# Optimization experiments

Measured on AMD Instinct MI355X. Metric: run time of the kernel, lower is better.

The kernel has to match this reference:

```python
import jax, jax.numpy as jnp
import numpy as np

B, F, CHUNK = 4096, 1024, 128  # batch, features, scan chunk size
EPS = 1e-5  # nn.LayerNorm default eps


def setup_inputs() -> dict:
    key = jax.random.key(0)
    k1, k2 = jax.random.split(key, 2)
    x = jax.random.normal(k1, (B, F), dtype=jnp.float32)
    W = jax.random.normal(k2, (F, F), dtype=jnp.float32) * 0.5  # init_weight = randn*0.5
    b = jnp.zeros((F,), dtype=jnp.float32)
    gamma = jnp.ones((F,), dtype=jnp.float32)   # LayerNorm weight
    beta = jnp.zeros((F,), dtype=jnp.float32)   # LayerNorm bias
    return {"x": x, "W": W, "b": b, "gamma": gamma, "beta": beta}


def reference(x, W, b, gamma, beta):
    # LayerNorm over last dim (biased variance, as torch)
    mu = jnp.mean(x, axis=-1, keepdims=True)
    var = jnp.mean(jnp.square(x - mu), axis=-1, keepdims=True)
    xn = (x - mu) * jax.lax.rsqrt(var + EPS) * gamma + beta  # [B, F]

    # Tropical max-plus matmul: out[b, i] = max_k xn[b, k] + W[k, i]
    # Chunk the batch to avoid materializing the full [B, F, F] broadcast-add.
    xc = xn.reshape(B // CHUNK, CHUNK, F)

    def step(_, xb):  # xb: [CHUNK, F]
        o = jnp.max(xb[:, :, None] + W[None, :, :], axis=1)  # [CHUNK, F]
        return None, o

    _, out = jax.lax.scan(step, None, xc)
    out = out.reshape(B, F)

    # Tropical bias: elementwise max with learned threshold b
    return jnp.maximum(out, b)
```

## Files before the change

kernel.cpp:

```cpp
#include <hip/hip_runtime.h>
#include <math.h>

#define F 1024
#define BM 256
#define BN 128
#define BK 16

typedef short s2 __attribute__((ext_vector_type(2)));
typedef short s4 __attribute__((ext_vector_type(4)));
typedef short s8 __attribute__((ext_vector_type(8)));
typedef float v4f __attribute__((ext_vector_type(4)));

#define SCALE 1024.0f
#define ISCALE (1.0f / 1024.0f)

static __device__ __forceinline__ s2 pk_max_i16(s2 a, s2 b) {
  s2 d;
  asm("v_pk_max_i16 %0, %1, %2" : "=v"(d) : "v"(a), "v"(b));
  return d;
}
static __device__ __forceinline__ s2 pk_add_blo(s2 a, s2 b) {
  s2 d;
  asm("v_pk_add_i16 %0, %1, %2 op_sel:[0,0] op_sel_hi:[0,1]" : "=v"(d) : "v"(a), "v"(b));
  return d;
}
static __device__ __forceinline__ s2 pk_add_bhi(s2 a, s2 b) {
  s2 d;
  asm("v_pk_add_i16 %0, %1, %2 op_sel:[1,0] op_sel_hi:[1,1]" : "=v"(d) : "v"(a), "v"(b));
  return d;
}

static __device__ __forceinline__ short q_i16(float v, float clampv) {
  return (short)__float2int_rn(fminf(fmaxf(v * SCALE, -clampv), clampv));
}

__global__ __launch_bounds__(256) void ln_kernel(const float* __restrict__ x,
                                                 const float* __restrict__ gamma,
                                                 const float* __restrict__ beta,
                                                 short* __restrict__ xn) {
  const int lane = threadIdx.x & 63;
  const int wv = threadIdx.x >> 6;
  const int row = blockIdx.x * 4 + wv;
  const float4* xr = (const float4*)(x + (size_t)row * F);
  float4 v[4];
  float s = 0.f;
#pragma unroll
  for (int j = 0; j < 4; ++j) {
    v[j] = xr[lane + 64 * j];
    s += v[j].x + v[j].y + v[j].z + v[j].w;
  }
#pragma unroll
  for (int off = 32; off; off >>= 1) s += __shfl_xor(s, off, 64);
  const float mu = s * (1.0f / F);
  float sq = 0.f;
#pragma unroll
  for (int j = 0; j < 4; ++j) {
    v[j].x -= mu; v[j].y -= mu; v[j].z -= mu; v[j].w -= mu;
    sq += v[j].x * v[j].x + v[j].y * v[j].y + v[j].z * v[j].z + v[j].w * v[j].w;
  }
#pragma unroll
  for (int off = 32; off; off >>= 1) sq += __shfl_xor(sq, off, 64);
  const float r = rsqrtf(sq * (1.0f / F) + 1e-5f);
  const float4* g4 = (const float4*)gamma;
  const float4* b4 = (const float4*)beta;
  s4* o = (s4*)(xn + (size_t)row * F);
#pragma unroll
  for (int j = 0; j < 4; ++j) {
    const int idx = lane + 64 * j;
    const float4 g = g4[idx];
    const float4 bb = b4[idx];
    s4 q;
    q[0] = q_i16(v[j].x * r * g.x + bb.x, 28000.f);
    q[1] = q_i16(v[j].y * r * g.y + bb.y, 28000.f);
    q[2] = q_i16(v[j].z * r * g.z + bb.z, 28000.f);
    q[3] = q_i16(v[j].w * r * g.w + bb.w, 28000.f);
    o[idx] = q;
  }
}

__global__ __launch_bounds__(256) void cvt_kernel(const float* __restrict__ Wf,
                                                  short* __restrict__ Wq) {
  const int i = blockIdx.x * 256 + threadIdx.x;
  const float4 v = ((const float4*)Wf)[i];
  s4 q;
  q[0] = q_i16(v.x, 4700.f);
  q[1] = q_i16(v.y, 4700.f);
  q[2] = q_i16(v.z, 4700.f);
  q[3] = q_i16(v.w, 4700.f);
  ((s4*)Wq)[i] = q;
}

__global__ __launch_bounds__(256, 2) void trop_i(const short* __restrict__ A,
                                                 const short* __restrict__ Wm,
                                                 const float* __restrict__ bias,
                                                 short* __restrict__ dsts,
                                                 float* __restrict__ outf,
                                                 int ntiles, int totrows, int fuse) {
  __shared__ alignas(16) short As[2][BK][BM];
  __shared__ alignas(16) short Bs[2][BK][BN];

  const int tid = threadIdx.x;
  const int tx = tid & 15;
  const int ty = tid >> 4;
  const int row0 = blockIdx.y * BM;
  const int col0 = blockIdx.x * BN;
  const int kbase = blockIdx.z * ntiles * BK;

  const int bk = tid >> 4;
  const int bn = (tid & 15) << 3;

  const short* Arow = A + (size_t)(row0 + tid) * F + kbase;
  const short* Wrow = Wm + (size_t)(kbase + bk) * F + col0 + bn;

  s2 acc[16][4];
  const s2 ninf = {(short)-32768, (short)-32768};
#pragma unroll
  for (int m = 0; m < 16; ++m)
#pragma unroll
    for (int n = 0; n < 4; ++n) acc[m][n] = ninf;

  {
    const s8 av0 = *(const s8*)Arow;
    const s8 av1 = *(const s8*)(Arow + 8);
    const s8 bv = *(const s8*)Wrow;
#pragma unroll
    for (int j = 0; j < 8; ++j) {
      As[0][j][tid] = av0[j];
      As[0][8 + j][tid] = av1[j];
    }
    *(s8*)&Bs[0][bk][bn] = bv;
  }
  __syncthreads();

  for (int kt = 0; kt < ntiles; ++kt) {
    const int cur = kt & 1;
    s8 av0, av1, bv;
    if (kt + 1 < ntiles) {
      const short* An = Arow + (kt + 1) * BK;
      av0 = *(const s8*)An;
      av1 = *(const s8*)(An + 8);
      bv = *(const s8*)(Wrow + (size_t)(kt + 1) * BK * F);
    }

#pragma unroll
    for (int k = 0; k < BK; ++k) {
      s8 alo = *(const s8*)&As[cur][k][ty * 16];
      s8 ahi = *(const s8*)&As[cur][k][ty * 16 + 8];
      s8 b = *(const s8*)&Bs[cur][k][tx * 8];
      const s2* al2 = (const s2*)&alo;
      const s2* ah2 = (const s2*)&ahi;
      const s2* b2 = (const s2*)&b;
#pragma unroll
      for (int m = 0; m < 8; ++m) {
        const s2 am = al2[m >> 1];
#pragma unroll
        for (int nn = 0; nn < 4; ++nn) {
          const s2 t = (m & 1) ? pk_add_bhi(am, b2[nn]) : pk_add_blo(am, b2[nn]);
          acc[m][nn] = pk_max_i16(acc[m][nn], t);
        }
      }
#pragma unroll
      for (int m = 0; m < 8; ++m) {
        const s2 am = ah2[m >> 1];
#pragma unroll
        for (int nn = 0; nn < 4; ++nn) {
          const s2 t = (m & 1) ? pk_add_bhi(am, b2[nn]) : pk_add_blo(am, b2[nn]);
          acc[8 + m][nn] = pk_max_i16(acc[8 + m][nn], t);
        }
      }
    }

    if (kt + 1 < ntiles) {
      const int nxt = cur ^ 1;
#pragma unroll
      for (int j = 0; j < 8; ++j) {
        As[nxt][j][tid] = av0[j];
        As[nxt][8 + j][tid] = av1[j];
      }
      *(s8*)&Bs[nxt][bk][bn] = bv;
      __syncthreads();
    }
  }

  if (fuse) {
    const float4 bv0 = *(const float4*)(bias + col0 + tx * 8);
    const float4 bv1 = *(const float4*)(bias + col0 + tx * 8 + 4);
#pragma unroll
    for (int m = 0; m < 16; ++m) {
      float* orow = outf + (size_t)(row0 + ty * 16 + m) * F + col0 + tx * 8;
      float4 o0, o1;
      o0.x = fmaxf((float)acc[m][0][0] * ISCALE, bv0.x);
      o0.y = fmaxf((float)acc[m][0][1] * ISCALE, bv0.y);
      o0.z = fmaxf((float)acc[m][1][0] * ISCALE, bv0.z);
      o0.w = fmaxf((float)acc[m][1][1] * ISCALE, bv0.w);
      o1.x = fmaxf((float)acc[m][2][0] * ISCALE, bv1.x);
      o1.y = fmaxf((float)acc[m][2][1] * ISCALE, bv1.y);
      o1.z = fmaxf((float)acc[m][3][0] * ISCALE, bv1.z);
      o1.w = fmaxf((float)acc[m][3][1] * ISCALE, bv1.w);
      *(float4*)orow = o0;
      *(float4*)(orow + 4) = o1;
    }
  } else {
    short* base = dsts + (size_t)blockIdx.z * totrows * F;
#pragma unroll
    for (int m = 0; m < 16; ++m) {
      short* orow = base + (size_t)(row0 + ty * 16 + m) * F + col0 + tx * 8;
      s8 o;
#pragma unroll
      for (int nn = 0; nn < 4; ++nn) {
        o[2 * nn] = acc[m][nn][0];
        o[2 * nn + 1] = acc[m][nn][1];
      }
      *(s8*)orow = o;
    }
  }
}

template <int NP>
__global__ __launch_bounds__(256) void combineNs(const short* __restrict__ p,
                                                 size_t plane,
                                                 const float* __restrict__ bias,
                                                 float* __restrict__ out) {
  const int i = blockIdx.x * 256 + threadIdx.x;
  s8 v = ((const s8*)p)[i];
  s2* vv = (s2*)&v;
#pragma unroll
  for (int q = 1; q < NP; ++q) {
    const s8 u = ((const s8*)(p + (size_t)q * plane))[i];
    const s2* uu = (const s2*)&u;
#pragma unroll
    for (int j = 0; j < 4; ++j) vv[j] = pk_max_i16(vv[j], uu[j]);
  }
  const int nb = (i & (F / 8 - 1)) * 8;
  const v4f bb0 = *(const v4f*)(bias + nb);
  const v4f bb1 = *(const v4f*)(bias + nb + 4);
  float4* o4 = (float4*)(out + (size_t)i * 8);
  float4 o0, o1;
  o0.x = fmaxf((float)v[0] * ISCALE, bb0.x);
  o0.y = fmaxf((float)v[1] * ISCALE, bb0.y);
  o0.z = fmaxf((float)v[2] * ISCALE, bb0.z);
  o0.w = fmaxf((float)v[3] * ISCALE, bb0.w);
  o1.x = fmaxf((float)v[4] * ISCALE, bb1.x);
  o1.y = fmaxf((float)v[5] * ISCALE, bb1.y);
  o1.z = fmaxf((float)v[6] * ISCALE, bb1.z);
  o1.w = fmaxf((float)v[7] * ISCALE, bb1.w);
  o4[0] = o0;
  o4[1] = o1;
}

extern "C" void kernel_launch(void* const* d_in, const int* in_sizes, int n_in,
                              void* d_out, int out_size, void* d_ws, size_t ws_size,
                              hipStream_t stream) {
  const float* x = (const float*)d_in[0];
  const float* Wm = (const float*)d_in[1];
  const float* bias = (const float*)d_in[2];
  const float* gamma = (const float*)d_in[3];
  const float* beta = (const float*)d_in[4];
  float* out = (float*)d_out;

  const int Brows = in_sizes[0] / F;
  const size_t plane = (size_t)Brows * F;

  short* xnq = (short*)d_ws;
  short* Wq = xnq + plane;
  short* parts = Wq + (size_t)F * F;

  ln_kernel<<<Brows / 4, 256, 0, stream>>>(x, gamma, beta, xnq);
  cvt_kernel<<<(F * F) / 1024, 256, 0, stream>>>(Wm, Wq);

  const size_t base2 = plane * 2 + (size_t)F * F * 2;
  const size_t need8 = base2 + 8 * plane * 2;
  const size_t need4 = base2 + 4 * plane * 2;
  const size_t need1 = base2;
  if (ws_size >= need8) {
    dim3 grid(F / BN, Brows / BM, 8);
    trop_i<<<grid, 256, 0, stream>>>(xnq, Wq, bias, parts, nullptr,
                                     (F / BK) / 8, Brows, 0);
    combineNs<8><<<(int)(plane / 2048), 256, 0, stream>>>(parts, plane, bias, out);
  } else if (ws_size >= need4) {
    dim3 grid(F / BN, Brows / BM, 4);
    trop_i<<<grid, 256, 0, stream>>>(xnq, Wq, bias, parts, nullptr,
                                     (F / BK) / 4, Brows, 0);
    combineNs<4><<<(int)(plane / 2048), 256, 0, stream>>>(parts, plane, bias, out);
  } else if (ws_size >= need1) {
    dim3 grid(F / BN, Brows / BM, 1);
    trop_i<<<grid, 256, 0, stream>>>(xnq, Wq, bias, nullptr, out, F / BK, Brows, 1);
  }
}
```

Measured before the change: 225.8 us.

## Transpose normalized activations and stage tiles via direct global-to-LDS loads

Adds a transpose kernel so the quantized activations are stored K-major. This lets the tropical matmul fill its shared-memory A and B tiles with global_load_lds 16-byte transfers, replacing register loads followed by scattered LDS stores. The goal is to cut register traffic and LDS store instructions in the main loop while keeping double buffering. The cost is an extra kernel launch, another pass over the activation plane, and a different workspace layout, with the partials buffer now aliasing the untransposed xn.

```diff
diff --git a/kernel.cpp b/kernel.cpp
--- a/kernel.cpp
+++ b/kernel.cpp
@@ -28,6 +28,12 @@
   s2 d;
   asm("v_pk_add_i16 %0, %1, %2 op_sel:[1,0] op_sel_hi:[1,1]" : "=v"(d) : "v"(a), "v"(b));
   return d;
+}
+
+static __device__ __forceinline__ void gll16(const short* src, short* lds) {
+  __builtin_amdgcn_global_load_lds(
+      (const __attribute__((address_space(1))) void*)src,
+      (__attribute__((address_space(3))) void*)lds, 16, 0, 0);
 }
 
 static __device__ __forceinline__ short q_i16(float v, float clampv) {
@@ -90,7 +96,32 @@
   ((s4*)Wq)[i] = q;
 }
 
-__global__ __launch_bounds__(256, 2) void trop_i(const short* __restrict__ A,
+__global__ __launch_bounds__(256) void tr_kernel(const short* __restrict__ xn,
+                                                 short* __restrict__ xnT,
+                                                 int Brows) {
+  __shared__ short t[64][72];
+  const int k0 = blockIdx.x * 64;
+  const int m0 = blockIdx.y * 64;
+  const int tid = threadIdx.x;
+  const int r = tid >> 3;
+  const int c = (tid & 7) << 3;
+#pragma unroll
+  for (int p = 0; p < 2; ++p) {
+    const int rr = r + p * 32;
+    *(s8*)&t[rr][c] = *(const s8*)&xn[(size_t)(m0 + rr) * F + k0 + c];
+  }
+  __syncthreads();
+#pragma unroll
+  for (int p = 0; p < 2; ++p) {
+    const int rr = r + p * 32;
+    s8 o;
+#pragma unroll
+    for (int j = 0; j < 8; ++j) o[j] = t[c + j][rr];
+    *(s8*)&xnT[(size_t)(k0 + rr) * Brows + m0 + c] = o;
+  }
+}
+
+__global__ __launch_bounds__(256, 2) void trop_i(const short* __restrict__ AT,
                                                  const short* __restrict__ Wm,
                                                  const float* __restrict__ bias,
                                                  short* __restrict__ dsts,
@@ -102,16 +133,12 @@
   const int tid = threadIdx.x;
   const int tx = tid & 15;
   const int ty = tid >> 4;
+  const int wv = tid >> 6;
+  const int lane = tid & 63;
   const int row0 = blockIdx.y * BM;
   const int col0 = blockIdx.x * BN;
   const int kbase = blockIdx.z * ntiles * BK;
 
-  const int bk = tid >> 4;
-  const int bn = (tid & 15) << 3;
-
-  const short* Arow = A + (size_t)(row0 + tid) * F + kbase;
-  const short* Wrow = Wm + (size_t)(kbase + bk) * F + col0 + bn;
-
   s2 acc[16][4];
   const s2 ninf = {(short)-32768, (short)-32768};
 #pragma unroll
@@ -119,28 +146,30 @@
 #pragma unroll
     for (int n = 0; n < 4; ++n) acc[m][n] = ninf;
 
-  {
-    const s8 av0 = *(const s8*)Arow;
-    const s8 av1 = *(const s8*)(Arow + 8);
-    const s8 bv = *(const s8*)Wrow;
-#pragma unroll
-    for (int j = 0; j < 8; ++j) {
-      As[0][j][tid] = av0[j];
-      As[0][8 + j][tid] = av1[j];
-    }
-    *(s8*)&Bs[0][bk][bn] = bv;
-  }
+#define STAGE(bufi, ktile)                                                     \
+  {                                                                            \
+    const int kb_ = kbase + (ktile) * BK;                                      \
+    _Pragma("unroll") for (int q = 0; q < 3; ++q) {                            \
+      const int i_ = wv * 3 + q;                                               \
+      if (i_ < 8) {                                                            \
+        const short* src_ = AT + (size_t)(kb_ + 2 * i_ + (lane >> 5)) * totrows\
+                            + row0 + ((lane & 31) << 3);                       \
+        gll16(src_, &As[bufi][2 * i_][0]);                                     \
+      } else {                                                                 \
+        const int cj_ = i_ - 8;                                                \
+        const short* src_ = Wm + (size_t)(kb_ + 4 * cj_ + (lane >> 4)) * F     \
+                            + col0 + ((lane & 15) << 3);                       \
+        gll16(src_, &Bs[bufi][4 * cj_][0]);                                    \
+      }                                                                        \
+    }                                                                          \
+  }
+
+  STAGE(0, 0);
   __syncthreads();
 
   for (int kt = 0; kt < ntiles; ++kt) {
     const int cur = kt & 1;
-    s8 av0, av1, bv;
-    if (kt + 1 < ntiles) {
-      const short* An = Arow + (kt + 1) * BK;
-      av0 = *(const s8*)An;
-      av1 = *(const s8*)(An + 8);
-      bv = *(const s8*)(Wrow + (size_t)(kt + 1) * BK * F);
-    }
+    if (kt + 1 < ntiles) STAGE(cur ^ 1, kt + 1);
 
 #pragma unroll
     for (int k = 0; k < BK; ++k) {
@@ -170,17 +199,9 @@
       }
     }
 
-    if (kt + 1 < ntiles) {
-      const int nxt = cur ^ 1;
-#pragma unroll
-      for (int j = 0; j < 8; ++j) {
-        As[nxt][j][tid] = av0[j];
-        As[nxt][8 + j][tid] = av1[j];
-      }
-      *(s8*)&Bs[nxt][bk][bn] = bv;
-      __syncthreads();
-    }
-  }
+    if (kt + 1 < ntiles) __syncthreads();
+  }
+#undef STAGE
 
   if (fuse) {
     const float4 bv0 = *(const float4*)(bias + col0 + tx * 8);
@@ -261,29 +282,34 @@
   const int Brows = in_sizes[0] / F;
   const size_t plane = (size_t)Brows * F;
 
-  short* xnq = (short*)d_ws;
-  short* Wq = xnq + plane;
-  short* parts = Wq + (size_t)F * F;
-
-  ln_kernel<<<Brows / 4, 256, 0, stream>>>(x, gamma, beta, xnq);
+  short* xnT = (short*)d_ws;
+  short* Wq = xnT + plane;
+  short* xn = Wq + (size_t)F * F;
+  short* parts = xn;
+
+  ln_kernel<<<Brows / 4, 256, 0, stream>>>(x, gamma, beta, xn);
   cvt_kernel<<<(F * F) / 1024, 256, 0, stream>>>(Wm, Wq);
-
-  const size_t base2 = plane * 2 + (size_t)F * F * 2;
-  const size_t need8 = base2 + 8 * plane * 2;
-  const size_t need4 = base2 + 4 * plane * 2;
+  {
+    dim3 tg(F / 64, Brows / 64);
+    tr_kernel<<<tg, 256, 0, stream>>>(xn, xnT, Brows);
+  }
+
+  const size_t base2 = 2 * plane * 2 + (size_t)F * F * 2;
+  const size_t need8 = plane * 2 + (size_t)F * F * 2 + 8 * plane * 2;
+  const size_t need4 = plane * 2 + (size_t)F * F * 2 + 4 * plane * 2;
   const size_t need1 = base2;
   if (ws_size >= need8) {
     dim3 grid(F / BN, Brows / BM, 8);
-    trop_i<<<grid, 256, 0, stream>>>(xnq, Wq, bias, parts, nullptr,
+    trop_i<<<grid, 256, 0, stream>>>(xnT, Wq, bias, parts, nullptr,
                                      (F / BK) / 8, Brows, 0);
     combineNs<8><<<(int)(plane / 2048), 256, 0, stream>>>(parts, plane, bias, out);
   } else if (ws_size >= need4) {
     dim3 grid(F / BN, Brows / BM, 4);
-    trop_i<<<grid, 256, 0, stream>>>(xnq, Wq, bias, parts, nullptr,
+    trop_i<<<grid, 256, 0, stream>>>(xnT, Wq, bias, parts, nullptr,
                                      (F / BK) / 4, Brows, 0);
     combineNs<4><<<(int)(plane / 2048), 256, 0, stream>>>(parts, plane, bias, out);
   } else if (ws_size >= need1) {
     dim3 grid(F / BN, Brows / BM, 1);
-    trop_i<<<grid, 256, 0, stream>>>(xnq, Wq, bias, nullptr, out, F / BK, Brows, 1);
-  }
-}
+    trop_i<<<grid, 256, 0, stream>>>(xnT, Wq, bias, nullptr, out, F / BK, Brows, 1);
+  }
+}
```

Result: slower. 232.8 us (+3.1%).
